# Optimization experiments

Measured on AMD Instinct MI355X. Metric: run time of the kernel, lower is better.

The kernel has to match this reference:

```python
import jax, jax.numpy as jnp
import numpy as np

B, C_IN, H, W = 16, 256, 64, 64
D, K = 128, 1024  # embed_dim, nb_entries


def setup_inputs() -> dict:
    key = jax.random.key(0)
    k1, k2, k3, k4 = jax.random.split(key, 4)
    x = jax.random.normal(k1, (B, C_IN, H, W), dtype=jnp.float32)
    conv_w = jax.random.normal(k2, (C_IN, D), dtype=jnp.float32) * 0.05
    conv_b = jax.random.normal(k3, (D,), dtype=jnp.float32) * 0.05
    embed = jax.random.normal(k4, (D, K), dtype=jnp.float32)
    return {"x": x, "conv_w": conv_w, "conv_b": conv_b, "embed": embed}


def reference(x, conv_w, conv_b, embed):
    # 1x1 conv == per-pixel matmul; go straight to NHWC layout.
    z = jnp.einsum('bchw,cd->bhwd', x, conv_w) + conv_b        # [B,H,W,D]
    flat = z.reshape(-1, D)                                     # [N,D]
    # Squared-euclidean distances to codebook columns (||f||^2 - 2 f.E + ||e||^2).
    dist = (jnp.sum(flat * flat, axis=1, keepdims=True)
            - 2.0 * (flat @ embed)
            + jnp.sum(embed * embed, axis=0, keepdims=True))    # [N,K]
    embed_ind = jnp.argmin(dist, axis=1)                        # [N] int
    embed_ind = embed_ind.reshape(B, H, W)
    quantize = jnp.take(embed.T, embed_ind, axis=0)             # [B,H,W,D] gather
    diff = jnp.mean((jax.lax.stop_gradient(quantize) - z) ** 2)
    quantize = z + jax.lax.stop_gradient(quantize - z)          # straight-through
    return quantize.transpose(0, 3, 1, 2), diff, embed_ind
```

## Files before the change

### kernel.cpp

```cpp
#include <hip/hip_runtime.h>

typedef __attribute__((ext_vector_type(4))) float f32x4;
typedef __attribute__((ext_vector_type(8))) short bf16x8;

constexpr int CIN = 256;
constexpr int D   = 128;
constexpr int K   = 1024;
constexpr int HW  = 4096;
constexpr int MT  = 128;
constexpr int DIFF_OFF = 8388608;
constexpr int IDX_OFF  = 8388609;

__device__ float g_scratch[16 + K];
__device__ __align__(16) uint4 g_efrags[64 * 4 * 64];
__device__ __align__(16) uint4 g_wfrags[8 * 8 * 3 * 64];
__device__ __align__(16) float g_embedT[K * D];

__device__ inline unsigned short f2bf(float f) {
    unsigned u = __float_as_uint(f);
    u = u + 0x7fff + ((u >> 16) & 1);
    return (unsigned short)(u >> 16);
}
__device__ inline float bf2f(unsigned short h) {
    return __uint_as_float(((unsigned)h) << 16);
}
__device__ inline void split3(float v, short& a, short& b, short& c) {
    unsigned short h = f2bf(v); float r1 = v - bf2f(h);
    unsigned short m = f2bf(r1); float r2 = r1 - bf2f(m);
    a = (short)h; b = (short)m; c = (short)f2bf(r2);
}
__device__ inline void split3t(float v, short& a, short& b, short& c) {
    unsigned u1 = __float_as_uint(v) & 0xffff0000u;
    float r1 = v - __uint_as_float(u1);
    unsigned u2 = __float_as_uint(r1) & 0xffff0000u;
    float r2 = r1 - __uint_as_float(u2);
    a = (short)(u1 >> 16); b = (short)(u2 >> 16);
    c = (short)(__float_as_uint(r2) >> 16);
}
__device__ inline float med3f(float a, float b, float c) {
    float d;
    asm("v_med3_f32 %0, %1, %2, %3" : "=v"(d) : "v"(a), "v"(b), "v"(c));
    return d;
}
__device__ inline float min3f(float a, float b, float c) {
    float d;
    asm("v_min3_f32 %0, %1, %2, %3" : "=v"(d) : "v"(a), "v"(b), "v"(c));
    return d;
}
__device__ inline float packk(float s, int kk) {
    return __uint_as_float((__float_as_uint(s) & 0xFFFFFC00u) | (unsigned)kk);
}

__device__ inline void gload_lds16(const uint4* g, uint4* l) {
    __builtin_amdgcn_global_load_lds(
        (const __attribute__((address_space(1))) unsigned int*)g,
        (__attribute__((address_space(3))) unsigned int*)l,
        16, 0, 0);
}

__global__ void vq_prep_all(const float* __restrict__ embed,
                            const float* __restrict__ conv_w) {
    const int bi = blockIdx.x;
    const int t  = threadIdx.x;
    if (bi < 128) {
        __shared__ float tile[32][33];
        int kb = bi >> 2, db = bi & 3;
        int tk = t & 31, td = t >> 5;
        #pragma unroll
        for (int dd = 0; dd < 4; ++dd)
            tile[td * 4 + dd][tk] =
                embed[(size_t)(db * 32 + td * 4 + dd) * K + kb * 32 + tk];
        __syncthreads();
        #pragma unroll
        for (int dd = 0; dd < 4; ++dd)
            g_embedT[(size_t)(kb * 32 + td * 4 + dd) * D + db * 32 + tk] =
                tile[tk][td * 4 + dd];
    } else if (bi < 192) {
        int kt = bi - 128, dc = t >> 6, l = t & 63;
        int k  = kt * 16 + (l & 15);
        int d0 = dc * 32 + (l >> 4) * 8;
        unsigned short hi[8];
        #pragma unroll
        for (int j = 0; j < 8; ++j)
            hi[j] = f2bf(embed[(size_t)(d0 + j) * K + k]);
        uint4 H;
        H.x = (unsigned)hi[0] | ((unsigned)hi[1] << 16);
        H.y = (unsigned)hi[2] | ((unsigned)hi[3] << 16);
        H.z = (unsigned)hi[4] | ((unsigned)hi[5] << 16);
        H.w = (unsigned)hi[6] | ((unsigned)hi[7] << 16);
        g_efrags[(kt * 4 + dc) * 64 + l] = H;
    } else if (bi < 208) {
        int old = (bi - 192) * 4 + (t >> 6), l = t & 63;
        int cb = old >> 3, db = old & 7;
        int c0 = cb * 32 + (l >> 4) * 8, d = db * 16 + (l & 15);
        short s1[8], s2[8], s3[8];
        #pragma unroll
        for (int j = 0; j < 8; ++j)
            split3(conv_w[(size_t)(c0 + j) * D + d], s1[j], s2[j], s3[j]);
        #pragma unroll
        for (int s = 0; s < 3; ++s) {
            const short* sp = s == 0 ? s1 : s == 1 ? s2 : s3;
            uint4 P;
            P.x = (unsigned)(unsigned short)sp[0] | ((unsigned)(unsigned short)sp[1] << 16);
            P.y = (unsigned)(unsigned short)sp[2] | ((unsigned)(unsigned short)sp[3] << 16);
            P.z = (unsigned)(unsigned short)sp[4] | ((unsigned)(unsigned short)sp[5] << 16);
            P.w = (unsigned)(unsigned short)sp[6] | ((unsigned)(unsigned short)sp[7] << 16);
            g_wfrags[((cb * 8 + db) * 3 + s) * 64 + l] = P;
        }
    } else {
        int k = (bi - 208) * 256 + t;
        if (k == 0) g_scratch[0] = 0.0f;
        float s = 0.0f;
        for (int d = 0; d < D; ++d) { float v = embed[d * K + k]; s += v * v; }
        g_scratch[16 + k] = s;
    }
}

#define MFMA(a, bb, c) __builtin_amdgcn_mfma_f32_16x16x32_bf16(a, bb, c, 0, 0, 0)

__global__ __launch_bounds__(256, 2) void vq_main(
    const float* __restrict__ x, const float* __restrict__ conv_b,
    float* __restrict__ out)
{
    __shared__ __align__(16) uint4 ebuf[4096];
    __shared__ float e2_s[K];
    __shared__ float tbuf[4 * 16 * 36];
    __shared__ int   ks_s[MT];
    __shared__ float red_s[4];

    const int t    = threadIdx.x;
    const int lane = t & 63;
    const int w    = t >> 6;
    const int wg   = blockIdx.x;
    const int n0   = wg * MT;
    const int b    = n0 >> 12;
    const int hw0  = n0 & 4095;
    const int pxb  = w * 32;
    const int lp   = lane & 15;
    const int lg   = lane >> 4;
    const float INF = __uint_as_float(0x7f800000u);

    for (int k = t; k < K; k += 256) e2_s[k] = g_scratch[16 + k];

    f32x4 Cz[2][8];
    #pragma unroll
    for (int db = 0; db < 8; ++db) {
        float bv = conv_b[db * 16 + lp];
        Cz[0][db] = (f32x4){bv, bv, bv, bv};
        Cz[1][db] = Cz[0][db];
    }
    {
        #pragma unroll
        for (int i = 0; i < 6; ++i)
            gload_lds16(&g_wfrags[(w * 6 + i) * 64 + lane], &ebuf[(w * 6 + i) * 64]);
        asm volatile("s_waitcnt vmcnt(0)" ::: "memory");
        __syncthreads();

        const float* xl = x + (size_t)b * CIN * HW + (size_t)(lg * 8) * HW
                          + hw0 + pxb + lp;
        for (int cb = 0; cb < 8; ++cb) {
            float v[2][8];
            #pragma unroll
            for (int rb = 0; rb < 2; ++rb)
                #pragma unroll
                for (int j = 0; j < 8; ++j)
                    v[rb][j] = xl[(size_t)(cb * 32 + j) * HW + rb * 16];
            if (cb < 7) {
                const uint4* wsrc = g_wfrags + (size_t)(cb + 1) * 1536;
                uint4* wdst = ebuf + ((cb + 1) & 1) * 1536;
                #pragma unroll
                for (int i = 0; i < 6; ++i)
                    gload_lds16(&wsrc[(w * 6 + i) * 64 + lane], &wdst[(w * 6 + i) * 64]);
            }
            bf16x8 X1[2], X2[2], X3[2];
            #pragma unroll
            for (int rb = 0; rb < 2; ++rb)
                #pragma unroll
                for (int j = 0; j < 8; ++j) {
                    short a, bb, c;
                    split3t(v[rb][j], a, bb, c);
                    X1[rb][j] = a; X2[rb][j] = bb; X3[rb][j] = c;
                }
            const uint4* wb = ebuf + (cb & 1) * 1536;
            #pragma unroll
            for (int db = 0; db < 8; ++db) {
                bf16x8 W1 = *(const bf16x8*)&wb[(db * 3 + 0) * 64 + lane];
                bf16x8 W2 = *(const bf16x8*)&wb[(db * 3 + 1) * 64 + lane];
                bf16x8 W3 = *(const bf16x8*)&wb[(db * 3 + 2) * 64 + lane];
                Cz[0][db] = MFMA(X1[0], W1, Cz[0][db]);
                Cz[1][db] = MFMA(X1[1], W1, Cz[1][db]);
                Cz[0][db] = MFMA(X1[0], W2, Cz[0][db]);
                Cz[1][db] = MFMA(X1[1], W2, Cz[1][db]);
                Cz[0][db] = MFMA(X2[0], W1, Cz[0][db]);
                Cz[1][db] = MFMA(X2[1], W1, Cz[1][db]);
                Cz[0][db] = MFMA(X1[0], W3, Cz[0][db]);
                Cz[1][db] = MFMA(X1[1], W3, Cz[1][db]);
                Cz[0][db] = MFMA(X2[0], W2, Cz[0][db]);
                Cz[1][db] = MFMA(X2[1], W2, Cz[1][db]);
                Cz[0][db] = MFMA(X3[0], W1, Cz[0][db]);
                Cz[1][db] = MFMA(X3[1], W1, Cz[1][db]);
            }
            asm volatile("s_waitcnt vmcnt(0)" ::: "memory");
            __syncthreads();
        }
    }

    bf16x8 A2h[2][4];
    {
        float* tb = tbuf + w * 576;
        #pragma unroll
        for (int rb = 0; rb < 2; ++rb) {
            #pragma unroll
            for (int dc = 0; dc < 4; ++dc) {
                #pragma unroll
                for (int h = 0; h < 2; ++h)
                    #pragma unroll
                    for (int r = 0; r < 4; ++r)
                        tb[(lg * 4 + r) * 36 + h * 16 + lp] = Cz[rb][dc * 2 + h][r];
                asm volatile("s_waitcnt lgkmcnt(0)" ::: "memory");
                f32x4 a0 = *(const f32x4*)&tb[lp * 36 + lg * 8];
                f32x4 a1 = *(const f32x4*)&tb[lp * 36 + lg * 8 + 4];
                #pragma unroll
                for (int j = 0; j < 8; ++j)
                    A2h[rb][dc][j] = (short)f2bf(-2.0f * (j < 4 ? a0[j] : a1[j - 4]));
                asm volatile("s_waitcnt lgkmcnt(0)" ::: "memory");
            }
        }
    }

    const uint4* gfr = g_efrags;
    {
        #pragma unroll
        for (int i = 0; i < 8; ++i)
            gload_lds16(&gfr[(w * 8 + i) * 64 + lane], &ebuf[(w * 8 + i) * 64]);
        asm volatile("s_waitcnt vmcnt(0)" ::: "memory");
        __syncthreads();
    }

    float v1[8], v2[8], v3[8], v4[8];
    #pragma unroll
    for (int q = 0; q < 8; ++q) { v1[q] = INF; v2[q] = INF; v3[q] = INF; v4[q] = INF; }

    for (int c = 0; c < 8; ++c) {
        if (c < 7) {
            const uint4* esrc = gfr + (size_t)(c + 1) * 2048;
            uint4* edst = ebuf + ((c + 1) & 1) * 2048;
            #pragma unroll
            for (int i = 0; i < 8; ++i)
                gload_lds16(&esrc[(w * 8 + i) * 64 + lane], &edst[(w * 8 + i) * 64]);
        }
        const bf16x8* eb = (const bf16x8*)&ebuf[(c & 1) * 2048];
        #pragma unroll
        for (int ktl = 0; ktl < 8; ++ktl) {
            int kt = c * 8 + ktl;
            bf16x8 Bh[4];
            #pragma unroll
            for (int dc = 0; dc < 4; ++dc)
                Bh[dc] = eb[(ktl * 4 + dc) * 64 + lane];
            float e2v = e2_s[kt * 16 + lp] + 512.0f;
            f32x4 C0 = (f32x4){e2v, e2v, e2v, e2v};
            f32x4 C1 = C0;
            __builtin_amdgcn_s_setprio(1);
            #pragma unroll
            for (int dc = 0; dc < 4; ++dc) {
                C0 = MFMA(A2h[0][dc], Bh[dc], C0);
                C1 = MFMA(A2h[1][dc], Bh[dc], C1);
            }
            __builtin_amdgcn_s_setprio(0);
            int kk = kt * 16 + lp;
            #pragma unroll
            for (int rb = 0; rb < 2; ++rb) {
                f32x4 C = rb ? C1 : C0;
                #pragma unroll
                for (int r = 0; r < 4; ++r) {
                    int q = rb * 4 + r;
                    float s = packk(C[r], kk);
                    float t1 = fminf(v1[q], s);
                    float t2 = med3f(s, v1[q], v2[q]);
                    float t3 = med3f(s, v2[q], v3[q]);
                    float t4 = med3f(s, v3[q], v4[q]);
                    v1[q] = t1; v2[q] = t2; v3[q] = t3; v4[q] = t4;
                }
            }
        }
        if (c < 7) asm volatile("s_waitcnt vmcnt(0)" ::: "memory");
        __syncthreads();
    }

    float dacc = 0.0f;
    #pragma unroll
    for (int q = 0; q < 8; ++q) {
        const int rb = q >> 2, r = q & 3;
        float a1 = v1[q], a2 = v2[q], a3 = v3[q], a4 = v4[q], a5 = INF, a6 = INF;
        #pragma unroll
        for (int off = 1; off < 16; off <<= 1) {
            float b1 = __shfl_xor(a1, off), b2 = __shfl_xor(a2, off);
            float b3 = __shfl_xor(a3, off), b4 = __shfl_xor(a4, off);
            float b5 = __shfl_xor(a5, off), b6 = __shfl_xor(a6, off);
            float m11 = fmaxf(a1, b1);
            float m12 = fmaxf(a1, b2), m21 = fmaxf(a2, b1);
            float m13 = fmaxf(a1, b3), m22 = fmaxf(a2, b2), m31 = fmaxf(a3, b1);
            float m14 = fmaxf(a1, b4), m23 = fmaxf(a2, b3), m32 = fmaxf(a3, b2), m41 = fmaxf(a4, b1);
            float m15 = fmaxf(a1, b5), m24 = fmaxf(a2, b4), m33 = fmaxf(a3, b3), m42 = fmaxf(a4, b2), m51 = fmaxf(a5, b1);
            float c1 = fminf(a1, b1);
            float c2 = min3f(a2, b2, m11);
            float c3 = min3f(m12, m21, fminf(a3, b3));
            float c4 = fminf(min3f(a4, b4, m13), fminf(m22, m31));
            float c5 = fminf(min3f(a5, b5, m14), min3f(m23, m32, m41));
            float c6 = fminf(fminf(min3f(a6, b6, m15), min3f(m24, m33, m42)), m51);
            a1 = c1; a2 = c2; a3 = c3; a4 = c4; a5 = c5; a6 = c6;
        }
        float cm[6] = {a1, a2, a3, a4, a5, a6};
        float bd = 0.0f; int bk = 0;
        #pragma unroll
        for (int j = 0; j < 6; ++j) {
            int kc = (int)(__float_as_uint(cm[j]) & 1023u);
            float sum = 0.0f;
            #pragma unroll
            for (int db = 0; db < 8; ++db)
                sum += Cz[rb][db][r] * g_embedT[(size_t)kc * D + db * 16 + lp];
            #pragma unroll
            for (int off = 1; off < 16; off <<= 1) sum += __shfl_xor(sum, off);
            float de = e2_s[kc] - 2.0f * sum;
            if (j == 0) { bd = de; bk = kc; }
            else {
                bool upd = (de < bd) || (de == bd && kc < bk);
                bd = upd ? de : bd;
                bk = upd ? kc : bk;
            }
        }
        #pragma unroll
        for (int db = 0; db < 8; ++db) {
            float qv = g_embedT[(size_t)bk * D + db * 16 + lp];
            float df = qv - Cz[rb][db][r];
            dacc += df * df;
        }
        if (lp == 0) {
            int px = pxb + rb * 16 + lg * 4 + r;
            ks_s[px] = bk;
            out[IDX_OFF + n0 + px] = (float)bk;
        }
    }
    #pragma unroll
    for (int off = 1; off <= 32; off <<= 1) dacc += __shfl_xor(dacc, off);
    if (lane == 0) red_s[w] = dacc;
    __syncthreads();

    {
        int px = t & 127, half = t >> 7;
        int ks = ks_s[px];
        const f32x4* ep = (const f32x4*)&g_embedT[(size_t)ks * D + half * 64];
        float* ob = out + (size_t)b * D * HW + hw0 + px;
        #pragma unroll
        for (int d4 = 0; d4 < 16; ++d4) {
            f32x4 q4 = ep[d4];
            int d = half * 64 + d4 * 4;
            #pragma unroll
            for (int cc = 0; cc < 4; ++cc)
                ob[(size_t)(d + cc) * HW] = q4[cc];
        }
    }
    if (t == 0) atomicAdd(&g_scratch[0], red_s[0] + red_s[1] + red_s[2] + red_s[3]);
}

__global__ void vq_final(float* __restrict__ out) {
    out[DIFF_OFF] = g_scratch[0] / 8388608.0f;
}

extern "C" void kernel_launch(void* const* d_in, const int* in_sizes, int n_in,
                              void* d_out, int out_size, void* d_ws, size_t ws_size,
                              hipStream_t stream) {
    const float* x      = (const float*)d_in[0];
    const float* conv_w = (const float*)d_in[1];
    const float* conv_b = (const float*)d_in[2];
    const float* embed  = (const float*)d_in[3];
    float* out = (float*)d_out;

    vq_prep_all<<<212, 256, 0, stream>>>(embed, conv_w);
    vq_main    <<<512, 256, 0, stream>>>(x, conv_b, out);
    vq_final   <<<1,   1,   0, stream>>>(out);
}
```

Before: 85.60 us.

## Read weight and codebook fragments directly from global memory instead of LDS staging

Removes the double-buffered LDS staging of the conv-weight and codebook MFMA fragments, along with the per-chunk barriers and waitcnts. Each lane now loads its bf16x8 fragments straight from global memory (served by L2/L1) inside the MFMA loops. This frees the 64KB ebuf of LDS, which could raise occupancy, and drops the synchronisation. The cost is exposed global-load latency on every fragment and no software prefetch ahead of the MFMAs.

New measurement: 93.69 us. +9.5%, slower.

```diff
diff --git a/kernel.cpp b/kernel.cpp
--- a/kernel.cpp
+++ b/kernel.cpp
@@ -49,13 +49,6 @@
 }
 __device__ inline float packk(float s, int kk) {
     return __uint_as_float((__float_as_uint(s) & 0xFFFFFC00u) | (unsigned)kk);
-}
-
-__device__ inline void gload_lds16(const uint4* g, uint4* l) {
-    __builtin_amdgcn_global_load_lds(
-        (const __attribute__((address_space(1))) unsigned int*)g,
-        (__attribute__((address_space(3))) unsigned int*)l,
-        16, 0, 0);
 }
 
 __global__ void vq_prep_all(const float* __restrict__ embed,
@@ -122,7 +115,6 @@
     const float* __restrict__ x, const float* __restrict__ conv_b,
     float* __restrict__ out)
 {
-    __shared__ __align__(16) uint4 ebuf[4096];
     __shared__ float e2_s[K];
     __shared__ float tbuf[4 * 16 * 36];
     __shared__ int   ks_s[MT];
@@ -150,14 +142,9 @@
         Cz[1][db] = Cz[0][db];
     }
     {
-        #pragma unroll
-        for (int i = 0; i < 6; ++i)
-            gload_lds16(&g_wfrags[(w * 6 + i) * 64 + lane], &ebuf[(w * 6 + i) * 64]);
-        asm volatile("s_waitcnt vmcnt(0)" ::: "memory");
-        __syncthreads();
-
         const float* xl = x + (size_t)b * CIN * HW + (size_t)(lg * 8) * HW
                           + hw0 + pxb + lp;
+        const bf16x8* wf = (const bf16x8*)g_wfrags;
         for (int cb = 0; cb < 8; ++cb) {
             float v[2][8];
             #pragma unroll
@@ -165,13 +152,6 @@
                 #pragma unroll
                 for (int j = 0; j < 8; ++j)
                     v[rb][j] = xl[(size_t)(cb * 32 + j) * HW + rb * 16];
-            if (cb < 7) {
-                const uint4* wsrc = g_wfrags + (size_t)(cb + 1) * 1536;
-                uint4* wdst = ebuf + ((cb + 1) & 1) * 1536;
-                #pragma unroll
-                for (int i = 0; i < 6; ++i)
-                    gload_lds16(&wsrc[(w * 6 + i) * 64 + lane], &wdst[(w * 6 + i) * 64]);
-            }
             bf16x8 X1[2], X2[2], X3[2];
             #pragma unroll
             for (int rb = 0; rb < 2; ++rb)
@@ -181,12 +161,11 @@
                     split3t(v[rb][j], a, bb, c);
                     X1[rb][j] = a; X2[rb][j] = bb; X3[rb][j] = c;
                 }
-            const uint4* wb = ebuf + (cb & 1) * 1536;
             #pragma unroll
             for (int db = 0; db < 8; ++db) {
-                bf16x8 W1 = *(const bf16x8*)&wb[(db * 3 + 0) * 64 + lane];
-                bf16x8 W2 = *(const bf16x8*)&wb[(db * 3 + 1) * 64 + lane];
-                bf16x8 W3 = *(const bf16x8*)&wb[(db * 3 + 2) * 64 + lane];
+                bf16x8 W1 = wf[((cb * 8 + db) * 3 + 0) * 64 + lane];
+                bf16x8 W2 = wf[((cb * 8 + db) * 3 + 1) * 64 + lane];
+                bf16x8 W3 = wf[((cb * 8 + db) * 3 + 2) * 64 + lane];
                 Cz[0][db] = MFMA(X1[0], W1, Cz[0][db]);
                 Cz[1][db] = MFMA(X1[1], W1, Cz[1][db]);
                 Cz[0][db] = MFMA(X1[0], W2, Cz[0][db]);
@@ -200,8 +179,6 @@
                 Cz[0][db] = MFMA(X3[0], W1, Cz[0][db]);
                 Cz[1][db] = MFMA(X3[1], W1, Cz[1][db]);
             }
-            asm volatile("s_waitcnt vmcnt(0)" ::: "memory");
-            __syncthreads();
         }
     }
 
@@ -228,63 +205,44 @@
         }
     }
 
-    const uint4* gfr = g_efrags;
-    {
-        #pragma unroll
-        for (int i = 0; i < 8; ++i)
-            gload_lds16(&gfr[(w * 8 + i) * 64 + lane], &ebuf[(w * 8 + i) * 64]);
-        asm volatile("s_waitcnt vmcnt(0)" ::: "memory");
-        __syncthreads();
-    }
+    __syncthreads();
 
     float v1[8], v2[8], v3[8], v4[8];
     #pragma unroll
     for (int q = 0; q < 8; ++q) { v1[q] = INF; v2[q] = INF; v3[q] = INF; v4[q] = INF; }
 
-    for (int c = 0; c < 8; ++c) {
-        if (c < 7) {
-            const uint4* esrc = gfr + (size_t)(c + 1) * 2048;
-            uint4* edst = ebuf + ((c + 1) & 1) * 2048;
-            #pragma unroll
-            for (int i = 0; i < 8; ++i)
-                gload_lds16(&esrc[(w * 8 + i) * 64 + lane], &edst[(w * 8 + i) * 64]);
-        }
-        const bf16x8* eb = (const bf16x8*)&ebuf[(c & 1) * 2048];
-        #pragma unroll
-        for (int ktl = 0; ktl < 8; ++ktl) {
-            int kt = c * 8 + ktl;
-            bf16x8 Bh[4];
-            #pragma unroll
-            for (int dc = 0; dc < 4; ++dc)
-                Bh[dc] = eb[(ktl * 4 + dc) * 64 + lane];
-            float e2v = e2_s[kt * 16 + lp] + 512.0f;
-            f32x4 C0 = (f32x4){e2v, e2v, e2v, e2v};
-            f32x4 C1 = C0;
-            __builtin_amdgcn_s_setprio(1);
-            #pragma unroll
-            for (int dc = 0; dc < 4; ++dc) {
-                C0 = MFMA(A2h[0][dc], Bh[dc], C0);
-                C1 = MFMA(A2h[1][dc], Bh[dc], C1);
+    const bf16x8* ef = (const bf16x8*)g_efrags;
+    #pragma unroll 2
+    for (int kt = 0; kt < 64; ++kt) {
+        bf16x8 Bh[4];
+        #pragma unroll
+        for (int dc = 0; dc < 4; ++dc)
+            Bh[dc] = ef[(kt * 4 + dc) * 64 + lane];
+        float e2v = e2_s[kt * 16 + lp] + 512.0f;
+        f32x4 C0 = (f32x4){e2v, e2v, e2v, e2v};
+        f32x4 C1 = C0;
+        __builtin_amdgcn_s_setprio(1);
+        #pragma unroll
+        for (int dc = 0; dc < 4; ++dc) {
+            C0 = MFMA(A2h[0][dc], Bh[dc], C0);
+            C1 = MFMA(A2h[1][dc], Bh[dc], C1);
+        }
+        __builtin_amdgcn_s_setprio(0);
+        int kk = kt * 16 + lp;
+        #pragma unroll
+        for (int rb = 0; rb < 2; ++rb) {
+            f32x4 C = rb ? C1 : C0;
+            #pragma unroll
+            for (int r = 0; r < 4; ++r) {
+                int q = rb * 4 + r;
+                float s = packk(C[r], kk);
+                float t1 = fminf(v1[q], s);
+                float t2 = med3f(s, v1[q], v2[q]);
+                float t3 = med3f(s, v2[q], v3[q]);
+                float t4 = med3f(s, v3[q], v4[q]);
+                v1[q] = t1; v2[q] = t2; v3[q] = t3; v4[q] = t4;
             }
-            __builtin_amdgcn_s_setprio(0);
-            int kk = kt * 16 + lp;
-            #pragma unroll
-            for (int rb = 0; rb < 2; ++rb) {
-                f32x4 C = rb ? C1 : C0;
-                #pragma unroll
-                for (int r = 0; r < 4; ++r) {
-                    int q = rb * 4 + r;
-                    float s = packk(C[r], kk);
-                    float t1 = fminf(v1[q], s);
-                    float t2 = med3f(s, v1[q], v2[q]);
-                    float t3 = med3f(s, v2[q], v3[q]);
-                    float t4 = med3f(s, v3[q], v4[q]);
-                    v1[q] = t1; v2[q] = t2; v3[q] = t3; v4[q] = t4;
-                }
-            }
-        }
-        if (c < 7) asm volatile("s_waitcnt vmcnt(0)" ::: "memory");
-        __syncthreads();
+        }
     }
 
     float dacc = 0.0f;
```

## Prefetch x register tiles, overlap codebook load, fold final kernel into last block

Applied to the files above, without the earlier changes.

The conv loop now double-buffers the x input in registers, so the next channel block's global loads are issued before the current block's split and MFMA work. The first codebook-fragment LDS load is moved ahead of the A-fragment transpose to overlap with it. The trailing barrier of the last codebook chunk is dropped. The separate vq_final launch is replaced by a last-block-done counter that writes the mean diff. This adds register pressure under launch_bounds(256,2) and relies on atomic and fence ordering for the final write.

Result: slower. 101.3 us (+18.4%).

```diff
diff --git a/kernel.cpp b/kernel.cpp
--- a/kernel.cpp
+++ b/kernel.cpp
@@ -12,6 +12,7 @@
 constexpr int IDX_OFF  = 8388609;
 
 __device__ float g_scratch[16 + K];
+__device__ int   g_done;
 __device__ __align__(16) uint4 g_efrags[64 * 4 * 64];
 __device__ __align__(16) uint4 g_wfrags[8 * 8 * 3 * 64];
 __device__ __align__(16) float g_embedT[K * D];
@@ -109,7 +110,7 @@
         }
     } else {
         int k = (bi - 208) * 256 + t;
-        if (k == 0) g_scratch[0] = 0.0f;
+        if (k == 0) { g_scratch[0] = 0.0f; g_done = 0; }
         float s = 0.0f;
         for (int d = 0; d < D; ++d) { float v = embed[d * K + k]; s += v * v; }
         g_scratch[16 + k] = s;
@@ -150,22 +151,29 @@
         Cz[1][db] = Cz[0][db];
     }
     {
+        const float* xl = x + (size_t)b * CIN * HW + (size_t)(lg * 8) * HW
+                          + hw0 + pxb + lp;
+
+        float vA[2][8], vB[2][8];
+        #pragma unroll
+        for (int rb = 0; rb < 2; ++rb)
+            #pragma unroll
+            for (int j = 0; j < 8; ++j)
+                vA[rb][j] = xl[(size_t)j * HW + rb * 16];
+
         #pragma unroll
         for (int i = 0; i < 6; ++i)
             gload_lds16(&g_wfrags[(w * 6 + i) * 64 + lane], &ebuf[(w * 6 + i) * 64]);
         asm volatile("s_waitcnt vmcnt(0)" ::: "memory");
         __syncthreads();
 
-        const float* xl = x + (size_t)b * CIN * HW + (size_t)(lg * 8) * HW
-                          + hw0 + pxb + lp;
-        for (int cb = 0; cb < 8; ++cb) {
-            float v[2][8];
-            #pragma unroll
-            for (int rb = 0; rb < 2; ++rb)
-                #pragma unroll
-                for (int j = 0; j < 8; ++j)
-                    v[rb][j] = xl[(size_t)(cb * 32 + j) * HW + rb * 16];
+        auto conv_step = [&](float (&vcur)[2][8], float (&vnext)[2][8], int cb) {
             if (cb < 7) {
+                #pragma unroll
+                for (int rb = 0; rb < 2; ++rb)
+                    #pragma unroll
+                    for (int j = 0; j < 8; ++j)
+                        vnext[rb][j] = xl[(size_t)((cb + 1) * 32 + j) * HW + rb * 16];
                 const uint4* wsrc = g_wfrags + (size_t)(cb + 1) * 1536;
                 uint4* wdst = ebuf + ((cb + 1) & 1) * 1536;
                 #pragma unroll
@@ -178,7 +186,7 @@
                 #pragma unroll
                 for (int j = 0; j < 8; ++j) {
                     short a, bb, c;
-                    split3t(v[rb][j], a, bb, c);
+                    split3t(vcur[rb][j], a, bb, c);
                     X1[rb][j] = a; X2[rb][j] = bb; X3[rb][j] = c;
                 }
             const uint4* wb = ebuf + (cb & 1) * 1536;
@@ -202,8 +210,17 @@
             }
             asm volatile("s_waitcnt vmcnt(0)" ::: "memory");
             __syncthreads();
-        }
-    }
+        };
+        for (int cb2 = 0; cb2 < 8; cb2 += 2) {
+            conv_step(vA, vB, cb2);
+            conv_step(vB, vA, cb2 + 1);
+        }
+    }
+
+    const uint4* gfr = g_efrags;
+    #pragma unroll
+    for (int i = 0; i < 8; ++i)
+        gload_lds16(&gfr[(w * 8 + i) * 64 + lane], &ebuf[(w * 8 + i) * 64]);
 
     bf16x8 A2h[2][4];
     {
@@ -227,15 +244,8 @@
             }
         }
     }
-
-    const uint4* gfr = g_efrags;
-    {
-        #pragma unroll
-        for (int i = 0; i < 8; ++i)
-            gload_lds16(&gfr[(w * 8 + i) * 64 + lane], &ebuf[(w * 8 + i) * 64]);
-        asm volatile("s_waitcnt vmcnt(0)" ::: "memory");
-        __syncthreads();
-    }
+    asm volatile("s_waitcnt vmcnt(0)" ::: "memory");
+    __syncthreads();
 
     float v1[8], v2[8], v3[8], v4[8];
     #pragma unroll
@@ -283,8 +293,10 @@
                 }
             }
         }
-        if (c < 7) asm volatile("s_waitcnt vmcnt(0)" ::: "memory");
-        __syncthreads();
+        if (c < 7) {
+            asm volatile("s_waitcnt vmcnt(0)" ::: "memory");
+            __syncthreads();
+        }
     }
 
     float dacc = 0.0f;
@@ -360,11 +372,14 @@
                 ob[(size_t)(d + cc) * HW] = q4[cc];
         }
     }
-    if (t == 0) atomicAdd(&g_scratch[0], red_s[0] + red_s[1] + red_s[2] + red_s[3]);
-}
-
-__global__ void vq_final(float* __restrict__ out) {
-    out[DIFF_OFF] = g_scratch[0] / 8388608.0f;
+    if (t == 0) {
+        atomicAdd(&g_scratch[0], red_s[0] + red_s[1] + red_s[2] + red_s[3]);
+        __threadfence();
+        if (atomicAdd(&g_done, 1) == 511) {
+            float v = atomicAdd(&g_scratch[0], 0.0f);
+            out[DIFF_OFF] = v * (1.0f / 8388608.0f);
+        }
+    }
 }
 
 extern "C" void kernel_launch(void* const* d_in, const int* in_sizes, int n_in,
@@ -378,5 +393,4 @@
 
     vq_prep_all<<<212, 256, 0, stream>>>(embed, conv_w);
     vq_main    <<<512, 256, 0, stream>>>(x, conv_b, out);
-    vq_final   <<<1,   1,   0, stream>>>(out);
-}
+}
```
